# Kernel optimization log

Measured on AMD Instinct MI355X. Metric: run time of the kernel, lower is better.

## Reference

```python
import jax, jax.numpy as jnp
import numpy as np

H = 1024
B = 8
S = 2048

def setup_inputs() -> dict:
    key = jax.random.key(0)
    ks = jax.random.split(key, 16)
    w = lambda k, shp: (jax.random.normal(k, shp, dtype=jnp.float32) * 0.02)
    return {
        "hidden_states": jax.random.normal(ks[0], (B, S, H), dtype=jnp.float32),
        "context_vector": jax.random.normal(ks[1], (B, H), dtype=jnp.float32),
        # nn.Linear weights stored torch-style as [out, in]
        "Wq": w(ks[2], (H, H)), "bq": w(ks[3], (H,)),
        "Wk": w(ks[4], (H, H)), "bk": w(ks[5], (H,)),
        "Wv": w(ks[6], (H, H)), "bv": w(ks[7], (H,)),
        "Wcq": w(ks[8], (H, H)),  # only .weight.t() used in original (no bias)
        "Wck": w(ks[9], (H, H)),
        "g_qh": jax.random.normal(ks[10], (H, 1), dtype=jnp.float32),
        "g_kh": jax.random.normal(ks[11], (H, 1), dtype=jnp.float32),
        "g_qc": jax.random.normal(ks[12], (H, 1), dtype=jnp.float32),
        "g_kc": jax.random.normal(ks[13], (H, 1), dtype=jnp.float32),
    }

def reference(hidden_states, context_vector, Wq, bq, Wk, bk, Wv, bv, Wcq, Wck, g_qh, g_kh, g_qc, g_kc):
    # Linear projections (torch Linear: x @ W.T + b)
    query = jnp.einsum('bsh,oh->bso', hidden_states, Wq) + bq   # [B,S,H]
    key_  = jnp.einsum('bsh,oh->bso', hidden_states, Wk) + bk
    value = jnp.einsum('bsh,oh->bso', hidden_states, Wv) + bv

    # gate = sigmoid(Q @ g_h + (ctx @ g_c)[:,None,:])  -> [B,S,1]
    q_gate = jax.nn.sigmoid(query @ g_qh + (context_vector @ g_qc)[:, None, :])
    k_gate = jax.nn.sigmoid(key_  @ g_kh + (context_vector @ g_kc)[:, None, :])

    # context projections: ctx @ weight.t() (no bias in original usage) -> [B,1,H]
    ctx_q = (context_vector @ Wcq.T)[:, None, :]
    ctx_k = (context_vector @ Wck.T)[:, None, :]

    query_hat = (1.0 - q_gate) * query + q_gate * ctx_q
    key_hat   = (1.0 - k_gate) * key_  + k_gate * ctx_k

    scale = 1.0 / jnp.sqrt(jnp.asarray(H, dtype=jnp.float32))
    scores = jnp.einsum('bqh,bkh->bqk', query_hat, key_hat) * scale  # [B,S,S]
    probs = jax.nn.softmax(scores, axis=-1)
    output = jnp.einsum('bqk,bkh->bqh', probs, value)  # [B,S,H]
    return (output, scores)
```

## Files before the change

### kernel.cpp

```cpp
#include <hip/hip_runtime.h>
#include <cstdint>
#include <cstddef>

#define H 1024
#define NB 8
#define S 2048
#define MROWS (NB*S)

using short8 = __attribute__((ext_vector_type(8))) short;
using f32x4  = __attribute__((ext_vector_type(4))) float;

__device__ __forceinline__ unsigned short f2bf(float f){
  union { float f; unsigned int u; } c; c.f = f;
  unsigned int u = c.u;
  return (unsigned short)((u + 0x7fffu + ((u >> 16) & 1u)) >> 16);
}


__global__ void k_cvt_bf16(const float* __restrict__ src, unsigned short* __restrict__ dst, int n){
  int i = (blockIdx.x * blockDim.x + threadIdx.x) * 4;
  if (i >= n) return;
  float4 v = *reinterpret_cast<const float4*>(src + i);
  ushort4 o;
  o.x = f2bf(v.x); o.y = f2bf(v.y); o.z = f2bf(v.z); o.w = f2bf(v.w);
  *reinterpret_cast<ushort4*>(dst + i) = o;
}

__global__ void k_colproj(const float* __restrict__ Wa, const float* __restrict__ ga, float* __restrict__ ua,
                          const float* __restrict__ Wb, const float* __restrict__ gb, float* __restrict__ ub){
  const float* W = blockIdx.y ? Wb : Wa;
  const float* g = blockIdx.y ? gb : ga;
  float* u = blockIdx.y ? ub : ua;
  int in = blockIdx.x * 256 + threadIdx.x;
  float s = 0.f;
  for (int o = 0; o < H; ++o) s = fmaf(W[(size_t)o * H + in], g[o], s);
  u[in] = s;
}

__global__ __launch_bounds__(256) void k_ctxproj(const float* __restrict__ Wcq, const float* __restrict__ Wck,
    const float* __restrict__ ctx, float* __restrict__ outq, float* __restrict__ outk){
  __shared__ float cs[NB * H];
  const float* W = blockIdx.y ? Wck : Wcq;
  float* out = blockIdx.y ? outk : outq;
  const int t = threadIdx.x;
  for (int i = t; i < NB * H; i += 256) cs[i] = ctx[i];
  __syncthreads();
  const int wid = t >> 6, lane = t & 63;
  const int row = blockIdx.x * 4 + wid;
  float a[NB];
  #pragma unroll
  for (int b = 0; b < NB; ++b) a[b] = 0.f;
  for (int i0 = 0; i0 < H; i0 += 64){
    const float w = W[(size_t)row * H + i0 + lane];
    #pragma unroll
    for (int b = 0; b < NB; ++b) a[b] = fmaf(w, cs[b * H + i0 + lane], a[b]);
  }
  #pragma unroll
  for (int b = 0; b < NB; ++b){
    float v = a[b];
    #pragma unroll
    for (int off = 32; off > 0; off >>= 1) v += __shfl_xor(v, off);
    if (lane == 0) out[b * H + row] = v;
  }
}

__device__ float block_dot(const float* a, const float* b, float* red, int t){
  float s = 0.f;
  for (int i = t; i < H; i += 256) s = fmaf(a[i], b[i], s);
  red[t] = s;
  __syncthreads();
  for (int off = 128; off > 0; off >>= 1){
    if (t < off) red[t] += red[t + off];
    __syncthreads();
  }
  float r = red[0];
  __syncthreads();
  return r;
}

__global__ void k_scalars(const float* __restrict__ bq, const float* __restrict__ gqh,
                          const float* __restrict__ bk, const float* __restrict__ gkh,
                          const float* __restrict__ ctx, const float* __restrict__ gqc,
                          const float* __restrict__ gkc, float* __restrict__ scal){
  __shared__ float red[256];
  const int t = threadIdx.x;
  float v;
  v = block_dot(bq, gqh, red, t); if (t == 0) scal[0] = v;
  v = block_dot(bk, gkh, red, t); if (t == 0) scal[1] = v;
  for (int b = 0; b < NB; ++b){
    v = block_dot(ctx + b * H, gqc, red, t); if (t == 0) scal[2 + b] = v;
    v = block_dot(ctx + b * H, gkc, red, t); if (t == 0) scal[10 + b] = v;
  }
}

__global__ __launch_bounds__(256) void k_prepass(const float* __restrict__ hs,
    const float* __restrict__ u_q, const float* __restrict__ u_k, const float* __restrict__ scal,
    unsigned short* __restrict__ hsb, float* __restrict__ gq, float* __restrict__ gk){
  const int t = threadIdx.x, wid = t >> 6, lane = t & 63;
  const int row = blockIdx.x * 4 + wid;
  const float* hrow = hs + (size_t)row * H;
  unsigned short* orow = hsb + (size_t)row * H;
  float sq = 0.f, sk = 0.f;
  #pragma unroll
  for (int c = 0; c < 4; ++c){
    const int idx = (lane + c * 64) * 4;
    float4 v  = *reinterpret_cast<const float4*>(hrow + idx);
    float4 uq = *reinterpret_cast<const float4*>(u_q + idx);
    float4 uk = *reinterpret_cast<const float4*>(u_k + idx);
    ushort4 o; o.x = f2bf(v.x); o.y = f2bf(v.y); o.z = f2bf(v.z); o.w = f2bf(v.w);
    *reinterpret_cast<ushort4*>(orow + idx) = o;
    sq += v.x*uq.x + v.y*uq.y + v.z*uq.z + v.w*uq.w;
    sk += v.x*uk.x + v.y*uk.y + v.z*uk.z + v.w*uk.w;
  }
  #pragma unroll
  for (int off = 32; off > 0; off >>= 1){
    sq += __shfl_xor(sq, off);
    sk += __shfl_xor(sk, off);
  }
  if (lane == 0){
    const int b = row >> 11;
    gq[row] = 1.f / (1.f + __expf(-(sq + scal[0] + scal[2 + b])));
    gk[row] = 1.f / (1.f + __expf(-(sk + scal[1] + scal[10 + b])));
  }
}

template<int MODE>
__global__ __launch_bounds__(256, 2)
void k_gemm(const unsigned short* __restrict__ A, const unsigned short* __restrict__ B,
            int K, int ldA, int ldB, long long Abatch, long long Bbatch,
            const float* __restrict__ gate, const float* __restrict__ bias,
            const float* __restrict__ ctxv,
            unsigned short* __restrict__ outb, float* __restrict__ outf,
            long long outBatch, float scale)
{
  constexpr int SMEM_SHORTS = (MODE == 2) ? (128 * 129) : (128 * 64 * 2);
  __shared__ __align__(16) short smem[SMEM_SHORTS];
  short* As = smem;
  short* Bs = smem + 128 * 64;

  const int t = threadIdx.x;
  const int wid = t >> 6;
  const int lane = t & 63;
  const int bz = blockIdx.z;
  const unsigned short* Ab = A + (size_t)bz * (size_t)Abatch;
  const unsigned short* Bb = B + (size_t)bz * (size_t)Bbatch;
  const int row0 = blockIdx.x * 128;
  const int col0 = blockIdx.y * 128;
  const int wr = (wid >> 1) * 64;
  const int wc = (wid & 1) * 64;

  f32x4 acc[4][4] = {};

  const int nk = K >> 6;
  for (int kt = 0; kt < nk; ++kt){
    const int k0 = kt << 6;
    #pragma unroll
    for (int i = 0; i < 4; ++i){
      const int c   = (wid * 4 + i) * 64 + lane;
      const int r   = c >> 3;
      const int sl  = c & 7;
      const int kcg = sl ^ (r & 7);
      const unsigned short* ga = Ab + (size_t)(row0 + r) * ldA + k0 + kcg * 8;
      const unsigned short* gb = Bb + (size_t)(col0 + r) * ldB + k0 + kcg * 8;
      __builtin_amdgcn_global_load_lds(
        (const __attribute__((address_space(1))) void*)ga,
        (__attribute__((address_space(3))) void*)((char*)As + (wid * 4 + i) * 1024),
        16, 0, 0);
      __builtin_amdgcn_global_load_lds(
        (const __attribute__((address_space(1))) void*)gb,
        (__attribute__((address_space(3))) void*)((char*)Bs + (wid * 4 + i) * 1024),
        16, 0, 0);
    }
    __syncthreads();
    #pragma unroll
    for (int kk = 0; kk < 2; ++kk){
      short8 af[4], bfr[4];
      #pragma unroll
      for (int m = 0; m < 4; ++m){
        const int ar = wr + m * 16 + (lane & 15);
        const int sl = ((kk * 4) + (lane >> 4)) ^ (ar & 7);
        af[m] = *reinterpret_cast<const short8*>((const char*)As + ar * 128 + sl * 16);
      }
      #pragma unroll
      for (int n = 0; n < 4; ++n){
        const int br = wc + n * 16 + (lane & 15);
        const int sl = ((kk * 4) + (lane >> 4)) ^ (br & 7);
        bfr[n] = *reinterpret_cast<const short8*>((const char*)Bs + br * 128 + sl * 16);
      }
      #pragma unroll
      for (int m = 0; m < 4; ++m)
        #pragma unroll
        for (int n = 0; n < 4; ++n)
          acc[m][n] = __builtin_amdgcn_mfma_f32_16x16x32_bf16(af[m], bfr[n], acc[m][n], 0, 0, 0);
    }
    __syncthreads();
  }

  if constexpr (MODE == 0 || MODE == 1){
    const int b = row0 >> 11;
    #pragma unroll
    for (int m = 0; m < 4; ++m)
      #pragma unroll
      for (int n = 0; n < 4; ++n)
        #pragma unroll
        for (int r = 0; r < 4; ++r){
          const int grow = row0 + wr + m * 16 + (lane >> 4) * 4 + r;
          const int gcol = col0 + wc + n * 16 + (lane & 15);
          const float g = gate[grow];
          const float q = acc[m][n][r] + bias[gcol];
          const float o = (1.f - g) * q + g * ctxv[b * H + gcol];
          outb[(size_t)grow * H + gcol] = f2bf(o);
        }
  } else if constexpr (MODE == 2){
    #pragma unroll
    for (int m = 0; m < 4; ++m)
      #pragma unroll
      for (int n = 0; n < 4; ++n)
        #pragma unroll
        for (int r = 0; r < 4; ++r){
          const int lr = wr + m * 16 + (lane >> 4) * 4 + r;
          const int lc = wc + n * 16 + (lane & 15);
          smem[lr * 129 + lc] = (short)f2bf(acc[m][n][r] + bias[col0 + lc]);
        }
    __syncthreads();
    const int bb = row0 >> 11;
    const int s0 = row0 & (S - 1);
    const int hl = t >> 1;
    const int sb = (t & 1) * 64;
    unsigned short* vout = outb + (size_t)bb * H * S + (size_t)(col0 + hl) * S + s0 + sb;
    #pragma unroll
    for (int i = 0; i < 64; i += 4){
      ushort4 o;
      o.x = (unsigned short)smem[(sb + i + 0) * 129 + hl];
      o.y = (unsigned short)smem[(sb + i + 1) * 129 + hl];
      o.z = (unsigned short)smem[(sb + i + 2) * 129 + hl];
      o.w = (unsigned short)smem[(sb + i + 3) * 129 + hl];
      *reinterpret_cast<ushort4*>(vout + i) = o;
    }
  } else if constexpr (MODE == 3){
    #pragma unroll
    for (int m = 0; m < 4; ++m)
      #pragma unroll
      for (int n = 0; n < 4; ++n)
        #pragma unroll
        for (int r = 0; r < 4; ++r){
          const int grow = row0 + wr + m * 16 + (lane >> 4) * 4 + r;
          const int gcol = col0 + wc + n * 16 + (lane & 15);
          outf[(size_t)bz * (size_t)outBatch + (size_t)grow * S + gcol] = acc[m][n][r] * scale;
        }
  } else {
    #pragma unroll
    for (int m = 0; m < 4; ++m)
      #pragma unroll
      for (int n = 0; n < 4; ++n)
        #pragma unroll
        for (int r = 0; r < 4; ++r){
          const int grow = row0 + wr + m * 16 + (lane >> 4) * 4 + r;
          const int gcol = col0 + wc + n * 16 + (lane & 15);
          outf[(size_t)bz * (size_t)outBatch + (size_t)grow * H + gcol] = acc[m][n][r];
        }
  }
}

__global__ __launch_bounds__(256) void k_softmax(const float* __restrict__ scores,
                                                 unsigned short* __restrict__ probs){
  const int row = blockIdx.x;
  const float* srow = scores + (size_t)row * S;
  unsigned short* prow = probs + (size_t)row * S;
  const int t = threadIdx.x, wid = t >> 6, lane = t & 63;
  __shared__ float red[8];
  float4 v0 = *reinterpret_cast<const float4*>(srow + t * 4);
  float4 v1 = *reinterpret_cast<const float4*>(srow + 1024 + t * 4);
  float m = fmaxf(fmaxf(fmaxf(v0.x, v0.y), fmaxf(v0.z, v0.w)),
                  fmaxf(fmaxf(v1.x, v1.y), fmaxf(v1.z, v1.w)));
  #pragma unroll
  for (int off = 32; off > 0; off >>= 1) m = fmaxf(m, __shfl_xor(m, off));
  if (lane == 0) red[wid] = m;
  __syncthreads();
  m = fmaxf(fmaxf(red[0], red[1]), fmaxf(red[2], red[3]));
  float4 e0, e1;
  e0.x = __expf(v0.x - m); e0.y = __expf(v0.y - m); e0.z = __expf(v0.z - m); e0.w = __expf(v0.w - m);
  e1.x = __expf(v1.x - m); e1.y = __expf(v1.y - m); e1.z = __expf(v1.z - m); e1.w = __expf(v1.w - m);
  float s = (e0.x + e0.y + e0.z + e0.w) + (e1.x + e1.y + e1.z + e1.w);
  #pragma unroll
  for (int off = 32; off > 0; off >>= 1) s += __shfl_xor(s, off);
  if (lane == 0) red[4 + wid] = s;
  __syncthreads();
  s = (red[4] + red[5]) + (red[6] + red[7]);
  const float inv = 1.f / s;
  ushort4 o;
  o.x = f2bf(e0.x * inv); o.y = f2bf(e0.y * inv); o.z = f2bf(e0.z * inv); o.w = f2bf(e0.w * inv);
  *reinterpret_cast<ushort4*>(prow + t * 4) = o;
  o.x = f2bf(e1.x * inv); o.y = f2bf(e1.y * inv); o.z = f2bf(e1.z * inv); o.w = f2bf(e1.w * inv);
  *reinterpret_cast<ushort4*>(prow + 1024 + t * 4) = o;
}

extern "C" void kernel_launch(void* const* d_in, const int* in_sizes, int n_in,
                              void* d_out, int out_size, void* d_ws, size_t ws_size,
                              hipStream_t stream) {
  const float* hs  = (const float*)d_in[0];
  const float* ctx = (const float*)d_in[1];
  const float* Wq  = (const float*)d_in[2];
  const float* bq  = (const float*)d_in[3];
  const float* Wk  = (const float*)d_in[4];
  const float* bk  = (const float*)d_in[5];
  const float* Wv  = (const float*)d_in[6];
  const float* bv  = (const float*)d_in[7];
  const float* Wcq = (const float*)d_in[8];
  const float* Wck = (const float*)d_in[9];
  const float* gqh = (const float*)d_in[10];
  const float* gkh = (const float*)d_in[11];
  const float* gqc = (const float*)d_in[12];
  const float* gkc = (const float*)d_in[13];

  char* ws = (char*)d_ws;
  const size_t T = (size_t)MROWS * H * 2;
  unsigned short* hsb  = (unsigned short*)(ws);
  unsigned short* qhat = (unsigned short*)(ws + T);
  unsigned short* khat = (unsigned short*)(ws + 2 * T);
  unsigned short* vt   = (unsigned short*)(ws + 3 * T);
  unsigned short* wqb  = (unsigned short*)(ws + 4 * T);
  unsigned short* wkb  = (unsigned short*)(ws + 4 * T + 2097152);
  unsigned short* wvb  = (unsigned short*)(ws + 4 * T + 4194304);
  float* u_q  = (float*)(ws + 4 * T + 6291456);
  float* u_k  = u_q + H;
  float* ctxq = u_k + H;
  float* ctxk = ctxq + NB * H;
  float* gq   = ctxk + NB * H;
  float* gk   = gq + MROWS;
  float* scal = gk + MROWS;
  unsigned short* probs = (unsigned short*)ws;

  float* out_attn   = (float*)d_out;
  float* out_scores = out_attn + (size_t)MROWS * H;

  k_cvt_bf16<<<1024, 256, 0, stream>>>(Wq, wqb, H * H);
  k_cvt_bf16<<<1024, 256, 0, stream>>>(Wk, wkb, H * H);
  k_cvt_bf16<<<1024, 256, 0, stream>>>(Wv, wvb, H * H);
  k_colproj<<<dim3(4, 2), 256, 0, stream>>>(Wq, gqh, u_q, Wk, gkh, u_k);
  k_ctxproj<<<dim3(256, 2), 256, 0, stream>>>(Wcq, Wck, ctx, ctxq, ctxk);
  k_scalars<<<1, 256, 0, stream>>>(bq, gqh, bk, gkh, ctx, gqc, gkc, scal);
  k_prepass<<<MROWS / 4, 256, 0, stream>>>(hs, u_q, u_k, scal, hsb, gq, gk);

  k_gemm<0><<<dim3(128, 8, 1), 256, 0, stream>>>(hsb, wqb, 1024, 1024, 1024, 0, 0,
      gq, bq, ctxq, qhat, nullptr, 0, 1.f);
  k_gemm<1><<<dim3(128, 8, 1), 256, 0, stream>>>(hsb, wkb, 1024, 1024, 1024, 0, 0,
      gk, bk, ctxk, khat, nullptr, 0, 1.f);
  k_gemm<2><<<dim3(128, 8, 1), 256, 0, stream>>>(hsb, wvb, 1024, 1024, 1024, 0, 0,
      nullptr, bv, nullptr, vt, nullptr, 0, 1.f);

  k_gemm<3><<<dim3(16, 16, 8), 256, 0, stream>>>(qhat, khat, 1024, 1024, 1024,
      (long long)S * H, (long long)S * H, nullptr, nullptr, nullptr,
      nullptr, out_scores, (long long)S * S, 0.03125f);

  k_softmax<<<MROWS, 256, 0, stream>>>(out_scores, probs);

  k_gemm<4><<<dim3(16, 8, 8), 256, 0, stream>>>(probs, vt, 2048, 2048, 2048,
      (long long)S * S, (long long)H * S, nullptr, nullptr, nullptr,
      nullptr, out_attn, (long long)S * H, 1.f);
}
```

Before: 395.0 us.

## Rewrite GEMM as 256x256 tile, 512-thread double-buffered pipelined MFMA kernel

The GEMM kernel moves from 128x128 tiles with 256 threads and a single LDS buffer to 256x256 tiles with 512 threads (8 waves). Operand loads are double-buffered in LDS with async global-to-LDS copies interleaved between MFMA groups, using explicit vmcnt waits, barriers and setprio. The goal is to hide memory latency and raise data reuse per tile. The column-projection reduction is split across more blocks and combined afterwards, and the three weight conversions are merged into one launch. Risks are more register pressure from the 8x4 accumulator array, fewer blocks per GEMM (256 for the projection GEMMs), and lower occupancy.

```diff
diff --git a/kernel.cpp b/kernel.cpp
--- a/kernel.cpp
+++ b/kernel.cpp
@@ -17,24 +17,36 @@
 }
 
 
-__global__ void k_cvt_bf16(const float* __restrict__ src, unsigned short* __restrict__ dst, int n){
-  int i = (blockIdx.x * blockDim.x + threadIdx.x) * 4;
-  if (i >= n) return;
+__global__ void k_cvt3(const float* __restrict__ a, const float* __restrict__ b, const float* __restrict__ c,
+                       unsigned short* __restrict__ oa, unsigned short* __restrict__ ob, unsigned short* __restrict__ oc){
+  const float* src = blockIdx.y == 0 ? a : (blockIdx.y == 1 ? b : c);
+  unsigned short* dst = blockIdx.y == 0 ? oa : (blockIdx.y == 1 ? ob : oc);
+  int i = (blockIdx.x * 256 + threadIdx.x) * 4;
   float4 v = *reinterpret_cast<const float4*>(src + i);
   ushort4 o;
   o.x = f2bf(v.x); o.y = f2bf(v.y); o.z = f2bf(v.z); o.w = f2bf(v.w);
   *reinterpret_cast<ushort4*>(dst + i) = o;
 }
 
-__global__ void k_colproj(const float* __restrict__ Wa, const float* __restrict__ ga, float* __restrict__ ua,
-                          const float* __restrict__ Wb, const float* __restrict__ gb, float* __restrict__ ub){
-  const float* W = blockIdx.y ? Wb : Wa;
-  const float* g = blockIdx.y ? gb : ga;
-  float* u = blockIdx.y ? ub : ua;
-  int in = blockIdx.x * 256 + threadIdx.x;
+__global__ void k_colproj(const float* __restrict__ Wq_, const float* __restrict__ gq_,
+                          const float* __restrict__ Wk_, const float* __restrict__ gk_,
+                          float* __restrict__ up){
+  const float* W = blockIdx.z ? Wk_ : Wq_;
+  const float* g = blockIdx.z ? gk_ : gq_;
+  const int in = blockIdx.x * 256 + threadIdx.x;
+  const int o0 = blockIdx.y * 128;
   float s = 0.f;
-  for (int o = 0; o < H; ++o) s = fmaf(W[(size_t)o * H + in], g[o], s);
-  u[in] = s;
+  for (int o = 0; o < 128; ++o) s = fmaf(W[(size_t)(o0 + o) * H + in], g[o0 + o], s);
+  up[(blockIdx.z * 8 + blockIdx.y) * 1024 + in] = s;
+}
+
+__global__ void k_ucombine(const float* __restrict__ up, float* __restrict__ uq, float* __restrict__ uk){
+  int i = blockIdx.x * 256 + threadIdx.x;
+  int m = i >> 10, j = i & 1023;
+  float s = 0.f;
+  #pragma unroll
+  for (int c = 0; c < 8; ++c) s += up[(m * 8 + c) * 1024 + j];
+  (m ? uk : uq)[j] = s;
 }
 
 __global__ __launch_bounds__(256) void k_ctxproj(const float* __restrict__ Wcq, const float* __restrict__ Wck,
@@ -124,8 +136,37 @@
   }
 }
 
+
+#define STG(bufi, opi, halfi, koff, P0, P1) \
+  { __builtin_amdgcn_global_load_lds((const __attribute__((address_space(1))) void*)(P0 + (koff)), \
+      (__attribute__((address_space(3))) void*)((char*)(&lds[bufi][opi][halfi][0]) + (wid*2+0)*1024), 16, 0, 0); \
+    __builtin_amdgcn_global_load_lds((const __attribute__((address_space(1))) void*)(P1 + (koff)), \
+      (__attribute__((address_space(3))) void*)((char*)(&lds[bufi][opi][halfi][0]) + (wid*2+1)*1024), 16, 0, 0); }
+#define STG_A(bufi, halfi, koff) STG(bufi, 0, halfi, koff, sA0, sA1)
+#define STG_B(bufi, halfi, koff) STG(bufi, 1, halfi, koff, sB0, sB1)
+
+#define DS_A(bufi, ks, mh) \
+  { _Pragma("unroll") for (int m_ = 0; m_ < 4; ++m_){ \
+      const int ar_ = wr*128 + ((mh)*4 + m_)*16 + (lane & 15); \
+      const int sl_ = (lane >> 4) ^ ((ar_ >> 1) & 3); \
+      af[m_] = *reinterpret_cast<const short8*>(&lds[bufi][0][ks][ar_*32 + sl_*8]); } }
+#define DS_B(bufi, ks) \
+  { _Pragma("unroll") for (int n_ = 0; n_ < 4; ++n_){ \
+      const int br_ = wc*64 + n_*16 + (lane & 15); \
+      const int sl_ = (lane >> 4) ^ ((br_ >> 1) & 3); \
+      bf[n_] = *reinterpret_cast<const short8*>(&lds[bufi][1][ks][br_*32 + sl_*8]); } }
+#define MFMA16(mh) \
+  { __builtin_amdgcn_s_setprio(1); \
+    _Pragma("unroll") for (int m_ = 0; m_ < 4; ++m_) \
+      _Pragma("unroll") for (int n_ = 0; n_ < 4; ++n_) \
+        acc[(mh)*4 + m_][n_] = __builtin_amdgcn_mfma_f32_16x16x32_bf16(af[m_], bf[n_], acc[(mh)*4 + m_][n_], 0, 0, 0); \
+    __builtin_amdgcn_s_setprio(0); }
+#define VM4() asm volatile("s_waitcnt vmcnt(4)" ::: "memory");
+#define VM0() asm volatile("s_waitcnt vmcnt(0)" ::: "memory");
+#define BAR() { asm volatile("" ::: "memory"); __builtin_amdgcn_s_barrier(); asm volatile("" ::: "memory"); }
+
 template<int MODE>
-__global__ __launch_bounds__(256, 2)
+__global__ __launch_bounds__(512, 2)
 void k_gemm(const unsigned short* __restrict__ A, const unsigned short* __restrict__ B,
             int K, int ldA, int ldB, long long Abatch, long long Bbatch,
             const float* __restrict__ gate, const float* __restrict__ bias,
@@ -133,131 +174,122 @@
             unsigned short* __restrict__ outb, float* __restrict__ outf,
             long long outBatch, float scale)
 {
-  constexpr int SMEM_SHORTS = (MODE == 2) ? (128 * 129) : (128 * 64 * 2);
-  __shared__ __align__(16) short smem[SMEM_SHORTS];
-  short* As = smem;
-  short* Bs = smem + 128 * 64;
+  __shared__ __align__(16) short lds[2][2][2][8192];
 
   const int t = threadIdx.x;
-  const int wid = t >> 6;
-  const int lane = t & 63;
+  const int wid = t >> 6, lane = t & 63;
+  const int wr = wid >> 2, wc = wid & 3;
   const int bz = blockIdx.z;
   const unsigned short* Ab = A + (size_t)bz * (size_t)Abatch;
   const unsigned short* Bb = B + (size_t)bz * (size_t)Bbatch;
-  const int row0 = blockIdx.x * 128;
-  const int col0 = blockIdx.y * 128;
-  const int wr = (wid >> 1) * 64;
-  const int wc = (wid & 1) * 64;
-
-  f32x4 acc[4][4] = {};
-
-  const int nk = K >> 6;
-  for (int kt = 0; kt < nk; ++kt){
-    const int k0 = kt << 6;
-    #pragma unroll
-    for (int i = 0; i < 4; ++i){
-      const int c   = (wid * 4 + i) * 64 + lane;
-      const int r   = c >> 3;
-      const int sl  = c & 7;
-      const int kcg = sl ^ (r & 7);
-      const unsigned short* ga = Ab + (size_t)(row0 + r) * ldA + k0 + kcg * 8;
-      const unsigned short* gb = Bb + (size_t)(col0 + r) * ldB + k0 + kcg * 8;
-      __builtin_amdgcn_global_load_lds(
-        (const __attribute__((address_space(1))) void*)ga,
-        (__attribute__((address_space(3))) void*)((char*)As + (wid * 4 + i) * 1024),
-        16, 0, 0);
-      __builtin_amdgcn_global_load_lds(
-        (const __attribute__((address_space(1))) void*)gb,
-        (__attribute__((address_space(3))) void*)((char*)Bs + (wid * 4 + i) * 1024),
-        16, 0, 0);
-    }
-    __syncthreads();
-    #pragma unroll
-    for (int kk = 0; kk < 2; ++kk){
-      short8 af[4], bfr[4];
-      #pragma unroll
-      for (int m = 0; m < 4; ++m){
-        const int ar = wr + m * 16 + (lane & 15);
-        const int sl = ((kk * 4) + (lane >> 4)) ^ (ar & 7);
-        af[m] = *reinterpret_cast<const short8*>((const char*)As + ar * 128 + sl * 16);
-      }
-      #pragma unroll
-      for (int n = 0; n < 4; ++n){
-        const int br = wc + n * 16 + (lane & 15);
-        const int sl = ((kk * 4) + (lane >> 4)) ^ (br & 7);
-        bfr[n] = *reinterpret_cast<const short8*>((const char*)Bs + br * 128 + sl * 16);
-      }
-      #pragma unroll
-      for (int m = 0; m < 4; ++m)
-        #pragma unroll
-        for (int n = 0; n < 4; ++n)
-          acc[m][n] = __builtin_amdgcn_mfma_f32_16x16x32_bf16(af[m], bfr[n], acc[m][n], 0, 0, 0);
-    }
-    __syncthreads();
+  const int row0 = blockIdx.x * 256;
+  const int col0 = blockIdx.y * 256;
+
+  const int c0 = (wid*2 + 0)*64 + lane;
+  const int c1 = (wid*2 + 1)*64 + lane;
+  const int r0s = c0 >> 2, r1s = c1 >> 2;
+  const int kc0 = (c0 & 3) ^ ((r0s >> 1) & 3);
+  const int kc1 = (c1 & 3) ^ ((r1s >> 1) & 3);
+  const unsigned short* sA0 = Ab + (size_t)(row0 + r0s) * (size_t)ldA + kc0*8;
+  const unsigned short* sA1 = Ab + (size_t)(row0 + r1s) * (size_t)ldA + kc1*8;
+  const unsigned short* sB0 = Bb + (size_t)(col0 + r0s) * (size_t)ldB + kc0*8;
+  const unsigned short* sB1 = Bb + (size_t)(col0 + r1s) * (size_t)ldB + kc1*8;
+
+  f32x4 acc[8][4] = {};
+  short8 af[4], bf[4];
+
+  STG_A(0, 0, 0); STG_B(0, 0, 0); STG_A(0, 1, 32); STG_B(0, 1, 32);
+  VM0(); BAR();
+
+  const int niter = K >> 7;
+  for (int it = 0; it < niter; ++it){
+    const int t1k = (it*2 + 1) << 6;
+    const int t2k = (it*2 + 2) << 6;
+    const bool more = (it + 1 < niter);
+    DS_A(0, 0, 0); DS_B(0, 0); STG_A(1, 0, t1k); MFMA16(0); BAR();
+    DS_A(0, 0, 1); STG_B(1, 0, t1k); MFMA16(1); VM4(); BAR();
+    DS_A(0, 1, 0); DS_B(0, 1); STG_A(1, 1, t1k + 32); MFMA16(0); BAR();
+    DS_A(0, 1, 1); STG_B(1, 1, t1k + 32); MFMA16(1);
+    if (more) { VM4(); } else { VM0(); }
+    BAR();
+    DS_A(1, 0, 0); DS_B(1, 0); if (more) STG_A(0, 0, t2k); MFMA16(0); BAR();
+    DS_A(1, 0, 1); if (more) { STG_B(0, 0, t2k); } MFMA16(1); if (more) VM4(); BAR();
+    DS_A(1, 1, 0); DS_B(1, 1); if (more) STG_A(0, 1, t2k + 32); MFMA16(0); BAR();
+    DS_A(1, 1, 1); if (more) { STG_B(0, 1, t2k + 32); } MFMA16(1); if (more) VM4(); BAR();
   }
 
   if constexpr (MODE == 0 || MODE == 1){
     const int b = row0 >> 11;
     #pragma unroll
-    for (int m = 0; m < 4; ++m)
+    for (int mi = 0; mi < 8; ++mi)
       #pragma unroll
       for (int n = 0; n < 4; ++n)
         #pragma unroll
         for (int r = 0; r < 4; ++r){
-          const int grow = row0 + wr + m * 16 + (lane >> 4) * 4 + r;
-          const int gcol = col0 + wc + n * 16 + (lane & 15);
+          const int grow = row0 + wr*128 + mi*16 + (lane >> 4)*4 + r;
+          const int gcol = col0 + wc*64 + n*16 + (lane & 15);
           const float g = gate[grow];
-          const float q = acc[m][n][r] + bias[gcol];
-          const float o = (1.f - g) * q + g * ctxv[b * H + gcol];
-          outb[(size_t)grow * H + gcol] = f2bf(o);
+          const float q = acc[mi][n][r] + bias[gcol];
+          outb[(size_t)grow * H + gcol] = f2bf((1.f - g) * q + g * ctxv[b * H + gcol]);
         }
   } else if constexpr (MODE == 2){
-    #pragma unroll
-    for (int m = 0; m < 4; ++m)
+    short* tp = (short*)lds;
+    const int bb = row0 >> 11;
+    const int s0 = row0 & (S - 1);
+    #pragma unroll
+    for (int ci = 0; ci < 2; ++ci)
+      #pragma unroll
+      for (int cj = 0; cj < 2; ++cj){
+        __syncthreads();
+        if (wr == ci && (wc >> 1) == cj){
+          const int lc0 = (wc & 1) * 64;
+          #pragma unroll
+          for (int mi = 0; mi < 8; ++mi)
+            #pragma unroll
+            for (int n = 0; n < 4; ++n)
+              #pragma unroll
+              for (int r = 0; r < 4; ++r){
+                const int lr = mi*16 + (lane >> 4)*4 + r;
+                const int lc = lc0 + n*16 + (lane & 15);
+                tp[lr*129 + lc] = (short)f2bf(acc[mi][n][r] + bias[col0 + cj*128 + lc]);
+              }
+        }
+        __syncthreads();
+        const int hl = t >> 2;
+        const int sb = (t & 3) * 32;
+        unsigned short* vout = outb + (size_t)bb * H * S + (size_t)(col0 + cj*128 + hl) * S
+                                    + (size_t)(s0 + ci*128 + sb);
+        #pragma unroll
+        for (int i2 = 0; i2 < 32; i2 += 4){
+          ushort4 o;
+          o.x = (unsigned short)tp[(sb + i2 + 0)*129 + hl];
+          o.y = (unsigned short)tp[(sb + i2 + 1)*129 + hl];
+          o.z = (unsigned short)tp[(sb + i2 + 2)*129 + hl];
+          o.w = (unsigned short)tp[(sb + i2 + 3)*129 + hl];
+          *reinterpret_cast<ushort4*>(vout + i2) = o;
+        }
+      }
+  } else if constexpr (MODE == 3){
+    #pragma unroll
+    for (int mi = 0; mi < 8; ++mi)
       #pragma unroll
       for (int n = 0; n < 4; ++n)
         #pragma unroll
         for (int r = 0; r < 4; ++r){
-          const int lr = wr + m * 16 + (lane >> 4) * 4 + r;
-          const int lc = wc + n * 16 + (lane & 15);
-          smem[lr * 129 + lc] = (short)f2bf(acc[m][n][r] + bias[col0 + lc]);
-        }
-    __syncthreads();
-    const int bb = row0 >> 11;
-    const int s0 = row0 & (S - 1);
-    const int hl = t >> 1;
-    const int sb = (t & 1) * 64;
-    unsigned short* vout = outb + (size_t)bb * H * S + (size_t)(col0 + hl) * S + s0 + sb;
-    #pragma unroll
-    for (int i = 0; i < 64; i += 4){
-      ushort4 o;
-      o.x = (unsigned short)smem[(sb + i + 0) * 129 + hl];
-      o.y = (unsigned short)smem[(sb + i + 1) * 129 + hl];
-      o.z = (unsigned short)smem[(sb + i + 2) * 129 + hl];
-      o.w = (unsigned short)smem[(sb + i + 3) * 129 + hl];
-      *reinterpret_cast<ushort4*>(vout + i) = o;
-    }
-  } else if constexpr (MODE == 3){
-    #pragma unroll
-    for (int m = 0; m < 4; ++m)
+          const int grow = row0 + wr*128 + mi*16 + (lane >> 4)*4 + r;
+          const int gcol = col0 + wc*64 + n*16 + (lane & 15);
+          outf[(size_t)bz * (size_t)outBatch + (size_t)grow * S + gcol] = acc[mi][n][r] * scale;
+        }
+  } else {
+    #pragma unroll
+    for (int mi = 0; mi < 8; ++mi)
       #pragma unroll
       for (int n = 0; n < 4; ++n)
         #pragma unroll
         for (int r = 0; r < 4; ++r){
-          const int grow = row0 + wr + m * 16 + (lane >> 4) * 4 + r;
-          const int gcol = col0 + wc + n * 16 + (lane & 15);
-          outf[(size_t)bz * (size_t)outBatch + (size_t)grow * S + gcol] = acc[m][n][r] * scale;
-        }
-  } else {
-    #pragma unroll
-    for (int m = 0; m < 4; ++m)
-      #pragma unroll
-      for (int n = 0; n < 4; ++n)
-        #pragma unroll
-        for (int r = 0; r < 4; ++r){
-          const int grow = row0 + wr + m * 16 + (lane >> 4) * 4 + r;
-          const int gcol = col0 + wc + n * 16 + (lane & 15);
-          outf[(size_t)bz * (size_t)outBatch + (size_t)grow * H + gcol] = acc[m][n][r];
+          const int grow = row0 + wr*128 + mi*16 + (lane >> 4)*4 + r;
+          const int gcol = col0 + wc*64 + n*16 + (lane & 15);
+          outf[(size_t)bz * (size_t)outBatch + (size_t)grow * H + gcol] = acc[mi][n][r];
         }
   }
 }
@@ -322,40 +354,41 @@
   unsigned short* wqb  = (unsigned short*)(ws + 4 * T);
   unsigned short* wkb  = (unsigned short*)(ws + 4 * T + 2097152);
   unsigned short* wvb  = (unsigned short*)(ws + 4 * T + 4194304);
-  float* u_q  = (float*)(ws + 4 * T + 6291456);
-  float* u_k  = u_q + H;
-  float* ctxq = u_k + H;
-  float* ctxk = ctxq + NB * H;
-  float* gq   = ctxk + NB * H;
-  float* gk   = gq + MROWS;
-  float* scal = gk + MROWS;
+  float* fb    = (float*)(ws + 4 * T + 6291456);
+  float* u_q   = fb;
+  float* u_k   = fb + 1024;
+  float* ctxq  = fb + 2048;
+  float* ctxk  = fb + 10240;
+  float* gq    = fb + 18432;
+  float* gk    = fb + 34816;
+  float* scal  = fb + 51200;
+  float* u_part= fb + 51232;
   unsigned short* probs = (unsigned short*)ws;
 
   float* out_attn   = (float*)d_out;
   float* out_scores = out_attn + (size_t)MROWS * H;
 
-  k_cvt_bf16<<<1024, 256, 0, stream>>>(Wq, wqb, H * H);
-  k_cvt_bf16<<<1024, 256, 0, stream>>>(Wk, wkb, H * H);
-  k_cvt_bf16<<<1024, 256, 0, stream>>>(Wv, wvb, H * H);
-  k_colproj<<<dim3(4, 2), 256, 0, stream>>>(Wq, gqh, u_q, Wk, gkh, u_k);
+  k_cvt3<<<dim3(1024, 3), 256, 0, stream>>>(Wq, Wk, Wv, wqb, wkb, wvb);
+  k_colproj<<<dim3(4, 8, 2), 256, 0, stream>>>(Wq, gqh, Wk, gkh, u_part);
+  k_ucombine<<<8, 256, 0, stream>>>(u_part, u_q, u_k);
   k_ctxproj<<<dim3(256, 2), 256, 0, stream>>>(Wcq, Wck, ctx, ctxq, ctxk);
   k_scalars<<<1, 256, 0, stream>>>(bq, gqh, bk, gkh, ctx, gqc, gkc, scal);
   k_prepass<<<MROWS / 4, 256, 0, stream>>>(hs, u_q, u_k, scal, hsb, gq, gk);
 
-  k_gemm<0><<<dim3(128, 8, 1), 256, 0, stream>>>(hsb, wqb, 1024, 1024, 1024, 0, 0,
+  k_gemm<0><<<dim3(64, 4, 1), 512, 0, stream>>>(hsb, wqb, 1024, 1024, 1024, 0, 0,
       gq, bq, ctxq, qhat, nullptr, 0, 1.f);
-  k_gemm<1><<<dim3(128, 8, 1), 256, 0, stream>>>(hsb, wkb, 1024, 1024, 1024, 0, 0,
+  k_gemm<1><<<dim3(64, 4, 1), 512, 0, stream>>>(hsb, wkb, 1024, 1024, 1024, 0, 0,
       gk, bk, ctxk, khat, nullptr, 0, 1.f);
-  k_gemm<2><<<dim3(128, 8, 1), 256, 0, stream>>>(hsb, wvb, 1024, 1024, 1024, 0, 0,
+  k_gemm<2><<<dim3(64, 4, 1), 512, 0, stream>>>(hsb, wvb, 1024, 1024, 1024, 0, 0,
       nullptr, bv, nullptr, vt, nullptr, 0, 1.f);
 
-  k_gemm<3><<<dim3(16, 16, 8), 256, 0, stream>>>(qhat, khat, 1024, 1024, 1024,
+  k_gemm<3><<<dim3(8, 8, 8), 512, 0, stream>>>(qhat, khat, 1024, 1024, 1024,
       (long long)S * H, (long long)S * H, nullptr, nullptr, nullptr,
       nullptr, out_scores, (long long)S * S, 0.03125f);
 
   k_softmax<<<MROWS, 256, 0, stream>>>(out_scores, probs);
 
-  k_gemm<4><<<dim3(16, 8, 8), 256, 0, stream>>>(probs, vt, 2048, 2048, 2048,
+  k_gemm<4><<<dim3(8, 4, 8), 512, 0, stream>>>(probs, vt, 2048, 2048, 2048,
       (long long)S * S, (long long)H * S, nullptr, nullptr, nullptr,
       nullptr, out_attn, (long long)S * H, 1.f);
 }
```

After: 357.0 us. -9.6%, faster.
